# Optimization experiments

Hardware: AMD Instinct MI355X
Metric: run time of the kernel (lower is better)

The kernel has to match this reference:

```python
import jax, jax.numpy as jnp
import numpy as np

N_MEL = 80


def _bce_with_logits(x, t):
    # mean over all elements, numerically stable
    return jnp.mean(jnp.maximum(x, 0.0) - x * t + jnp.log1p(jnp.exp(-jnp.abs(x))))


def _spectral_mel_loss(pred, target):
    w = np.ones(N_MEL, dtype=np.float32)
    w[N_MEL // 4: 3 * N_MEL // 4] *= 1.5
    w[3 * N_MEL // 4:] *= 0.8
    w = jnp.asarray(w)[None, :, None]
    weighted_mse = jnp.mean((pred * w - target * w) ** 2)
    l1 = jnp.mean(jnp.abs(pred - target))
    dp = pred[:, :, 1:] - pred[:, :, :-1]
    dt = target[:, :, 1:] - target[:, :, :-1]
    spectral = jnp.mean((dp - dt) ** 2)
    return weighted_mse + 0.3 * l1 + 0.2 * spectral


def _perceptual_loss(pred, target):
    fw = jnp.exp(-jnp.arange(N_MEL, dtype=jnp.float32) / 20.0)[None, :, None]
    weighted = ((pred - target) ** 2) * fw
    l1 = jnp.mean(jnp.abs(pred - target))
    return jnp.mean(weighted) + 0.5 * l1


def _style_loss(pred, target):
    mean_loss = jnp.mean((jnp.mean(pred, axis=2) - jnp.mean(target, axis=2)) ** 2)
    # torch.var defaults to unbiased (ddof=1)
    var_loss = jnp.mean((jnp.var(pred, axis=2, ddof=1) - jnp.var(target, axis=2, ddof=1)) ** 2)
    c, t = pred.shape[1], pred.shape[2]
    gram_p = jnp.einsum('bct,bdt->bcd', pred, pred) / (c * t)
    gram_t = jnp.einsum('bct,bdt->bcd', target, target) / (c * t)
    gram_loss = jnp.mean((gram_p - gram_t) ** 2)
    return mean_loss + var_loss + 0.5 * gram_loss


def _monotonic_loss(att):
    # att: [B, mel_len, text_len]; vectorized form of the per-step violation loop
    b, mel_len, _ = att.shape
    peaks = jnp.argmax(att, axis=2).astype(jnp.float32)  # [B, mel_len]
    viol = jnp.maximum(peaks[:, :-1] - peaks[:, 1:], 0.0)
    return jnp.sum(viol) / (b * mel_len)


def setup_inputs() -> dict:
    key = jax.random.key(0)
    ks = jax.random.split(key, 6)
    B, C, T, L = 64, N_MEL, 2000, 200
    return {
        'mel_out': jax.random.normal(ks[0], (B, C, T), jnp.float32),
        'mel_out_postnet': jax.random.normal(ks[1], (B, C, T), jnp.float32),
        'mel_target': jax.random.normal(ks[2], (B, C, T), jnp.float32),
        'gate_out': jax.random.normal(ks[3], (B, T), jnp.float32),
        'gate_target': jax.random.uniform(ks[4], (B, T), jnp.float32),
        'attention_weights': jax.random.uniform(ks[5], (B, T, L), jnp.float32),
    }


def reference(mel_out, mel_out_postnet, mel_target, gate_out, gate_target, attention_weights):
    # loss weights (hparams defaults); guide_loss omitted (method truncated in source)
    mel_w, gate_w, spec_w, perc_w, style_w, mono_w = 1.0, 1.0, 0.3, 0.2, 0.1, 0.1
    gate_inner_w = 1.3  # AdaptiveGateLoss initial_weight

    mel_loss = jnp.mean((mel_out - mel_target) ** 2) + jnp.mean((mel_out_postnet - mel_target) ** 2)
    gate_loss = gate_inner_w * _bce_with_logits(gate_out.reshape(-1, 1), gate_target.reshape(-1, 1))
    spectral = _spectral_mel_loss(mel_out_postnet, mel_target)
    perceptual = _perceptual_loss(mel_out_postnet, mel_target)
    style = _style_loss(mel_out_postnet, mel_target)
    mono = _monotonic_loss(attention_weights)

    total = (mel_w * mel_loss + gate_w * gate_loss + spec_w * spectral
             + perc_w * perceptual + style_w * style + mono_w * mono)
    return total
```

## Files before the change

### kernel.cpp

```cpp
#include <hip/hip_runtime.h>
#include <math.h>

#define N_MEL 80
#define B_    64
#define T_    2000
#define L_    200
#define ROWS   (B_*N_MEL)
#define NTOT   (B_*N_MEL*T_)
#define GATE_N (B_*T_)
#define ATT_ROWS (B_*T_)
#define AV_ROWS 64
#define NVIOL  (ATT_ROWS/AV_ROWS)

#define G_MELB   (ROWS/4)
#define G_GATE   64

#define WS_ROWPART 0
#define WS_M8      (WS_ROWPART + ROWS*8)
#define WS_GATEP   (WS_M8 + 8*64*6400)
#define WS_VIOLP   (WS_GATEP + 64)
#define WS_GFP     (WS_VIOLP + NVIOL)

typedef __attribute__((ext_vector_type(8)))  short bf16x8;
typedef __attribute__((ext_vector_type(16))) float f32x16;
typedef unsigned short ush;

__device__ __forceinline__ float blockReduceSum256(float v) {
    __shared__ float red[4];
    #pragma unroll
    for (int off = 32; off; off >>= 1) v += __shfl_down(v, off, 64);
    int lane = threadIdx.x & 63, w = threadIdx.x >> 6;
    if (lane == 0) red[w] = v;
    __syncthreads();
    if (threadIdx.x == 0) v = red[0] + red[1] + red[2] + red[3];
    return v;
}

__device__ __forceinline__ unsigned short f2bf(float f) {
    unsigned u = __float_as_uint(f);
    u = (u + 0x7fffu + ((u >> 16) & 1u)) >> 16;
    return (unsigned short)u;
}

__device__ __forceinline__ void merge4(float& b, int& p) {
    #pragma unroll
    for (int m = 1; m <= 2; m <<= 1) {
        float ob = __shfl_xor(b, m, 64);
        int   op = __shfl_xor(p, m, 64);
        if (ob > b || (ob == b && op < p)) { b = ob; p = op; }
    }
}

__device__ __forceinline__ void scan_sub(const float* __restrict__ rowp, int q,
                                         float& bOut, int& pOut) {
    const float4* rp = (const float4*)rowp;
    float4 v[13];
    #pragma unroll
    for (int i = 0; i < 12; i++) v[i] = rp[q + 4*i];
    v[12] = make_float4(-1.f, -1.f, -1.f, -1.f);
    if (q < 2) v[12] = rp[q + 48];
    float bx=-1.f, by=-1.f, bz=-1.f, bw=-1.f;
    int jx=0, jy=0, jz=0, jw=0;
    #pragma unroll
    for (int i = 0; i < 13; i++) {
        int j = q + 4*i;
        if (v[i].x > bx) { bx = v[i].x; jx = j; }
        if (v[i].y > by) { by = v[i].y; jy = j; }
        if (v[i].z > bz) { bz = v[i].z; jz = j; }
        if (v[i].w > bw) { bw = v[i].w; jw = j; }
    }
    float b = bx; int p = 4*jx;
    if (by > b || (by == b && 4*jy+1 < p)) { b = by; p = 4*jy+1; }
    if (bz > b || (bz == b && 4*jz+2 < p)) { b = bz; p = 4*jz+2; }
    if (bw > b || (bw == b && 4*jw+3 < p)) { b = bw; p = 4*jw+3; }
    bOut = b; pOut = p;
}

__global__ __launch_bounds__(256, 2) void k_melgate(const float* __restrict__ mo,
                                                    const float* __restrict__ mp,
                                                    const float* __restrict__ mt,
                                                    const float* __restrict__ gx,
                                                    const float* __restrict__ gt,
                                                    float* __restrict__ ws) {
    const int bid = blockIdx.x;
    float* rowpart = ws + WS_ROWPART;
    float* gatep   = ws + WS_GATEP;

    if (bid >= G_MELB) {
        const int gb = bid - G_MELB;
        const float4* x4 = (const float4*)gx;
        const float4* t4 = (const float4*)gt;
        float s = 0;
        for (int i = gb*256 + threadIdx.x; i < GATE_N/4; i += G_GATE*256) {
            float4 x = x4[i], t = t4[i];
            float xs[4] = {x.x, x.y, x.z, x.w}, ts[4] = {t.x, t.y, t.z, t.w};
            #pragma unroll
            for (int k = 0; k < 4; k++)
                s += fmaxf(xs[k], 0.0f) - xs[k]*ts[k] + log1pf(expf(-fabsf(xs[k])));
        }
        float tot = blockReduceSum256(s);
        if (threadIdx.x == 0) gatep[gb] = tot;
        return;
    }

    {
        const int wid  = threadIdx.x >> 6;
        const int lane = threadIdx.x & 63;
        const int row  = bid * 4 + wid;
        const long base = (long)row * T_;
        const float4* mo4 = (const float4*)(mo + base);
        const float4* mp4 = (const float4*)(mp + base);
        const float4* mt4 = (const float4*)(mt + base);

        float4 A[8], P[8], Q[8];
        #pragma unroll
        for (int k = 0; k < 7; k++) {
            A[k] = mo4[lane + 64*k];
            P[k] = mp4[lane + 64*k];
            Q[k] = mt4[lane + 64*k];
        }
        const bool t7 = (lane < 52);
        A[7] = make_float4(0.f,0.f,0.f,0.f);
        P[7] = make_float4(0.f,0.f,0.f,0.f);
        Q[7] = make_float4(0.f,0.f,0.f,0.f);
        if (t7) { A[7] = mo4[lane + 448]; P[7] = mp4[lane + 448]; Q[7] = mt4[lane + 448]; }

        float s1=0, s2=0, sl1=0, std_=0, sp=0, sp2=0, st=0, st2=0;
        float carry = 0.f;
        #pragma unroll
        for (int k = 0; k < 8; k++) {
            float4 a = A[k], p = P[k], t = Q[k];
            float e0=a.x-t.x, e1=a.y-t.y, e2=a.z-t.z, e3=a.w-t.w;
            s1 += e0*e0 + e1*e1 + e2*e2 + e3*e3;
            float d0=p.x-t.x, d1=p.y-t.y, d2=p.z-t.z, d3=p.w-t.w;
            s2 += d0*d0 + d1*d1 + d2*d2 + d3*d3;
            sl1 += fabsf(d0) + fabsf(d1) + fabsf(d2) + fabsf(d3);
            sp  += p.x + p.y + p.z + p.w;
            sp2 += p.x*p.x + p.y*p.y + p.z*p.z + p.w*p.w;
            st  += t.x + t.y + t.z + t.w;
            st2 += t.x*t.x + t.y*t.y + t.z*t.z + t.w*t.w;
            float q1 = d1-d0, q2 = d2-d1, q3 = d3-d2;
            std_ += q1*q1 + q2*q2 + q3*q3;
            float pv = __shfl_up(d3, 1, 64);
            if (lane == 0) pv = carry;
            float q0 = d0 - pv;
            bool valid = !(k == 0 && lane == 0) && (k < 7 || t7);
            if (valid) std_ += q0*q0;
            carry = __shfl(d3, 63, 64);
        }

        float vals[8] = {s1, s2, sl1, std_, sp, sp2, st, st2};
        #pragma unroll
        for (int k = 0; k < 8; k++) {
            float v = vals[k];
            #pragma unroll
            for (int off = 32; off; off >>= 1) v += __shfl_down(v, off, 64);
            vals[k] = v;
        }
        if (lane == 0) {
            *(float4*)&rowpart[row*8]     = make_float4(vals[0], vals[1], vals[2], vals[3]);
            *(float4*)&rowpart[row*8 + 4] = make_float4(vals[4], vals[5], vals[6], vals[7]);
        }
    }
}

__global__ __launch_bounds__(192) void k_gram(const float* __restrict__ mp,
                                              const float* __restrict__ mt,
                                              float* __restrict__ M8) {
    const int b  = blockIdx.x >> 3;
    const int kc = blockIdx.x & 7;
    const int k0 = kc * 256;
    const int NS = (kc < 7) ? 16 : 13;

    __shared__ ush Dls[2][96][24];
    __shared__ ush Sls[2][96][24];

    const int tid  = threadIdx.x;
    const int row  = tid >> 1;
    const int half = tid & 1;
    const int lane = tid & 63;
    const int wv   = tid >> 6;
    const long bbase = (long)b * (N_MEL * T_);
    const float* prow = mp + bbase + (long)row * T_ + k0 + half * 8;
    const float* trow = mt + bbase + (long)row * T_ + k0 + half * 8;
    const bool rv = (row < N_MEL);

    f32x16 acc0 = {}, acc1 = {}, acc2 = {};
    float4 pa0, pa1, ta0, ta1;

    auto loadreg = [&](int s) {
        if (rv) {
            pa0 = *(const float4*)(prow + s*16);
            pa1 = *(const float4*)(prow + s*16 + 4);
            ta0 = *(const float4*)(trow + s*16);
            ta1 = *(const float4*)(trow + s*16 + 4);
        } else {
            pa0 = pa1 = ta0 = ta1 = make_float4(0.f, 0.f, 0.f, 0.f);
        }
    };
    auto writelds = [&](int buf) {
        bf16x8 d, s;
        d[0]=f2bf(pa0.x-ta0.x); d[1]=f2bf(pa0.y-ta0.y); d[2]=f2bf(pa0.z-ta0.z); d[3]=f2bf(pa0.w-ta0.w);
        d[4]=f2bf(pa1.x-ta1.x); d[5]=f2bf(pa1.y-ta1.y); d[6]=f2bf(pa1.z-ta1.z); d[7]=f2bf(pa1.w-ta1.w);
        s[0]=f2bf(pa0.x+ta0.x); s[1]=f2bf(pa0.y+ta0.y); s[2]=f2bf(pa0.z+ta0.z); s[3]=f2bf(pa0.w+ta0.w);
        s[4]=f2bf(pa1.x+ta1.x); s[5]=f2bf(pa1.y+ta1.y); s[6]=f2bf(pa1.z+ta1.z); s[7]=f2bf(pa1.w+ta1.w);
        *(bf16x8*)&Dls[buf][row][half*8] = d;
        *(bf16x8*)&Sls[buf][row][half*8] = s;
    };

    loadreg(0);
    writelds(0);
    __syncthreads();

    const int frow = lane & 31;
    const int fkh  = lane >> 5;
    for (int s = 0; s < NS; s++) {
        const int cur = s & 1;
        if (s + 1 < NS) loadreg(s + 1);
        bf16x8 af = *(const bf16x8*)&Dls[cur][wv*32 + frow][fkh*8];
        bf16x8 b0 = *(const bf16x8*)&Sls[cur][      frow][fkh*8];
        bf16x8 b1 = *(const bf16x8*)&Sls[cur][ 32 + frow][fkh*8];
        bf16x8 b2 = *(const bf16x8*)&Sls[cur][ 64 + frow][fkh*8];
        acc0 = __builtin_amdgcn_mfma_f32_32x32x16_bf16(af, b0, acc0, 0, 0, 0);
        acc1 = __builtin_amdgcn_mfma_f32_32x32x16_bf16(af, b1, acc1, 0, 0, 0);
        acc2 = __builtin_amdgcn_mfma_f32_32x32x16_bf16(af, b2, acc2, 0, 0, 0);
        if (s + 1 < NS) writelds((s + 1) & 1);
        __syncthreads();
    }

    float* Mb = M8 + ((long)(kc * B_ + b)) * 6400;
    #pragma unroll
    for (int r = 0; r < 16; r++) {
        int row32 = (r & 3) + 8 * (r >> 2) + 4 * (lane >> 5);
        int c = wv * 32 + row32;
        if (c < N_MEL) {
            Mb[c*80 + frow]      = acc0[r];
            Mb[c*80 + 32 + frow] = acc1[r];
            if (frow < 16) Mb[c*80 + 64 + frow] = acc2[r];
        }
    }
}

__global__ __launch_bounds__(256) void k_gramfin(const float* __restrict__ ws_ro,
                                                 float* __restrict__ gfp) {
    __shared__ float Ms[N_MEL][N_MEL + 1];
    const float* M8 = ws_ro + WS_M8;
    const int b = blockIdx.x;
    const float inv = 1.0f / (float)(N_MEL * T_);

    for (int i = threadIdx.x; i < 6400; i += 256) {
        float m = 0.f;
        #pragma unroll
        for (int kc = 0; kc < 8; kc++)
            m += M8[((long)(kc * B_ + b)) * 6400 + i];
        Ms[i / N_MEL][i % N_MEL] = m;
    }
    __syncthreads();

    float s = 0.f;
    for (int i = threadIdx.x; i < 6400; i += 256) {
        int c = i / N_MEL, d = i % N_MEL;
        float g = 0.5f * (Ms[c][d] + Ms[d][c]) * inv;
        s += g * g;
    }
    float tot = blockReduceSum256(s);
    if (threadIdx.x == 0) gfp[b] = tot;
}

__global__ __launch_bounds__(256, 2) void k_argviol(const float* __restrict__ att,
                                                    float* __restrict__ ws) {
    float* violp = ws + WS_VIOLP;
    __shared__ float pk[AV_ROWS + 1];
    const int ab = blockIdx.x;
    const int g = threadIdx.x >> 2;
    const int q = threadIdx.x & 3;
    const int r0 = ab * AV_ROWS;
    const int r  = r0 + g;

    float b; int p;
    scan_sub(att + (long)r * L_, q, b, p);
    merge4(b, p);
    if (q == 0) pk[g] = (float)p;

    const int rb = r0 + AV_ROWS;
    const bool need_b = ((rb % T_) != 0) && (rb < ATT_ROWS);
    if (g == 0 && need_b) {
        float b2; int p2;
        scan_sub(att + (long)rb * L_, q, b2, p2);
        merge4(b2, p2);
        if (q == 0) pk[AV_ROWS] = (float)p2;
    }
    __syncthreads();

    float s = 0;
    if (threadIdx.x < AV_ROWS) {
        int rr = r0 + threadIdx.x;
        if (((rr + 1) % T_) != 0)
            s = fmaxf(pk[threadIdx.x] - pk[threadIdx.x + 1], 0.0f);
    }
    float tot = blockReduceSum256(s);
    if (threadIdx.x == 0) violp[ab] = tot;
}

__global__ __launch_bounds__(256) void k_final2(const float* __restrict__ ws_ro,
                                                float* __restrict__ out) {
    const float* rowpart = ws_ro + WS_ROWPART;
    const float* gatep   = ws_ro + WS_GATEP;
    const float* violp   = ws_ro + WS_VIOLP;
    const float* gfp     = ws_ro + WS_GFP;

    float a[11] = {0,0,0,0,0,0,0,0,0,0,0};
    for (int row = threadIdx.x; row < ROWS; row += 256) {
        const float4 lo = *(const float4*)(rowpart + row*8);
        const float4 hi = *(const float4*)(rowpart + row*8 + 4);
        int c = row % N_MEL;
        float wc = (c >= 3*N_MEL/4) ? 0.8f : ((c >= N_MEL/4) ? 1.5f : 1.0f);
        float fw = expf(-(float)c / 20.0f);
        a[0] += lo.x;
        a[1] += lo.y;
        a[2] += wc*wc*lo.y;
        a[3] += lo.z;
        a[4] += lo.w;
        a[5] += fw*lo.y;
        float md = (hi.x - hi.z) * (1.0f / T_);
        a[6] += md*md;
        float vp = (hi.y - hi.x*hi.x*(1.0f/T_)) * (1.0f/(T_-1));
        float vt = (hi.w - hi.z*hi.z*(1.0f/T_)) * (1.0f/(T_-1));
        float vd = vp - vt;
        a[7] += vd*vd;
    }
    for (int i = threadIdx.x; i < NVIOL; i += 256) a[9] += violp[i];
    if (threadIdx.x < 64) { a[8] = gatep[threadIdx.x]; a[10] = gfp[threadIdx.x]; }

    __shared__ float red[4][11];
    #pragma unroll
    for (int k = 0; k < 11; k++) {
        float v = a[k];
        #pragma unroll
        for (int off = 32; off; off >>= 1) v += __shfl_down(v, off, 64);
        a[k] = v;
    }
    int lane = threadIdx.x & 63, w = threadIdx.x >> 6;
    if (lane == 0) {
        #pragma unroll
        for (int k = 0; k < 11; k++) red[w][k] = a[k];
    }
    __syncthreads();
    if (threadIdx.x == 0) {
        float r[11];
        #pragma unroll
        for (int k = 0; k < 11; k++) r[k] = red[0][k] + red[1][k] + red[2][k] + red[3][k];
        const float invN = 1.0f / (float)NTOT;
        float mel        = (r[0] + r[1]) * invN;
        float gate       = 1.3f * r[8] / (float)GATE_N;
        float wmse       = r[2] * invN;
        float l1         = r[3] * invN;
        float sdiff      = r[4] / (float)(B_ * N_MEL * (T_ - 1));
        float spectral   = wmse + 0.3f*l1 + 0.2f*sdiff;
        float perceptual = r[5]*invN + 0.5f*l1;
        float mean_loss  = r[6] / (float)ROWS;
        float var_loss   = r[7] / (float)ROWS;
        float gram       = r[10] / (float)(B_ * 6400);
        float style      = mean_loss + var_loss + 0.5f*gram;
        float mono       = r[9] / (float)(B_ * T_);
        out[0] = mel + gate + 0.3f*spectral + 0.2f*perceptual + 0.1f*style + 0.1f*mono;
    }
}

extern "C" void kernel_launch(void* const* d_in, const int* in_sizes, int n_in,
                              void* d_out, int out_size, void* d_ws, size_t ws_size,
                              hipStream_t stream) {
    const float* mo  = (const float*)d_in[0];
    const float* mp  = (const float*)d_in[1];
    const float* mt  = (const float*)d_in[2];
    const float* gx  = (const float*)d_in[3];
    const float* gt  = (const float*)d_in[4];
    const float* att = (const float*)d_in[5];
    float* ws = (float*)d_ws;

    k_melgate<<<G_MELB + G_GATE, 256, 0, stream>>>(mo, mp, mt, gx, gt, ws);
    k_gram   <<<512,  192, 0, stream>>>(mp, mt, ws + WS_M8);
    k_gramfin<<<64,   256, 0, stream>>>(ws, ws + WS_GFP);
    k_argviol<<<NVIOL, 256, 0, stream>>>(att, ws);
    k_final2 <<<1,    256, 0, stream>>>(ws, (float*)d_out);
}
```

Baseline: 94.12 us.

## Fuse mel row statistics into gram MFMA kernel and gate BCE into argmax kernel

Removes the separate mel/gate pass, which read mel_out_postnet and mel_target a second time. The per-row sums are now accumulated inside the gram kernel while its tiles are loaded, and the gate BCE blocks move into the attention argmax launch. Per-chunk row partials go to a new workspace region and are summed in extra blocks of the gram-finalize kernel, which saves one launch and about 2 x 41 MB of HBM reads. In exchange, the gram kernel carries more registers and ALU work per step, and the spectral-difference term needs extra boundary handling across chunks.

```diff
diff --git a/kernel.cpp b/kernel.cpp
--- a/kernel.cpp
+++ b/kernel.cpp
@@ -12,11 +12,9 @@
 #define AV_ROWS 64
 #define NVIOL  (ATT_ROWS/AV_ROWS)
 
-#define G_MELB   (ROWS/4)
-#define G_GATE   64
-
 #define WS_ROWPART 0
-#define WS_M8      (WS_ROWPART + ROWS*8)
+#define WS_ROWCH   (WS_ROWPART + ROWS*8)
+#define WS_M8      (WS_ROWCH + 8*ROWS*8)
 #define WS_GATEP   (WS_M8 + 8*64*6400)
 #define WS_VIOLP   (WS_GATEP + 64)
 #define WS_GFP     (WS_VIOLP + NVIOL)
@@ -76,97 +74,12 @@
     bOut = b; pOut = p;
 }
 
-__global__ __launch_bounds__(256, 2) void k_melgate(const float* __restrict__ mo,
-                                                    const float* __restrict__ mp,
-                                                    const float* __restrict__ mt,
-                                                    const float* __restrict__ gx,
-                                                    const float* __restrict__ gt,
-                                                    float* __restrict__ ws) {
-    const int bid = blockIdx.x;
-    float* rowpart = ws + WS_ROWPART;
-    float* gatep   = ws + WS_GATEP;
-
-    if (bid >= G_MELB) {
-        const int gb = bid - G_MELB;
-        const float4* x4 = (const float4*)gx;
-        const float4* t4 = (const float4*)gt;
-        float s = 0;
-        for (int i = gb*256 + threadIdx.x; i < GATE_N/4; i += G_GATE*256) {
-            float4 x = x4[i], t = t4[i];
-            float xs[4] = {x.x, x.y, x.z, x.w}, ts[4] = {t.x, t.y, t.z, t.w};
-            #pragma unroll
-            for (int k = 0; k < 4; k++)
-                s += fmaxf(xs[k], 0.0f) - xs[k]*ts[k] + log1pf(expf(-fabsf(xs[k])));
-        }
-        float tot = blockReduceSum256(s);
-        if (threadIdx.x == 0) gatep[gb] = tot;
-        return;
-    }
-
-    {
-        const int wid  = threadIdx.x >> 6;
-        const int lane = threadIdx.x & 63;
-        const int row  = bid * 4 + wid;
-        const long base = (long)row * T_;
-        const float4* mo4 = (const float4*)(mo + base);
-        const float4* mp4 = (const float4*)(mp + base);
-        const float4* mt4 = (const float4*)(mt + base);
-
-        float4 A[8], P[8], Q[8];
-        #pragma unroll
-        for (int k = 0; k < 7; k++) {
-            A[k] = mo4[lane + 64*k];
-            P[k] = mp4[lane + 64*k];
-            Q[k] = mt4[lane + 64*k];
-        }
-        const bool t7 = (lane < 52);
-        A[7] = make_float4(0.f,0.f,0.f,0.f);
-        P[7] = make_float4(0.f,0.f,0.f,0.f);
-        Q[7] = make_float4(0.f,0.f,0.f,0.f);
-        if (t7) { A[7] = mo4[lane + 448]; P[7] = mp4[lane + 448]; Q[7] = mt4[lane + 448]; }
-
-        float s1=0, s2=0, sl1=0, std_=0, sp=0, sp2=0, st=0, st2=0;
-        float carry = 0.f;
-        #pragma unroll
-        for (int k = 0; k < 8; k++) {
-            float4 a = A[k], p = P[k], t = Q[k];
-            float e0=a.x-t.x, e1=a.y-t.y, e2=a.z-t.z, e3=a.w-t.w;
-            s1 += e0*e0 + e1*e1 + e2*e2 + e3*e3;
-            float d0=p.x-t.x, d1=p.y-t.y, d2=p.z-t.z, d3=p.w-t.w;
-            s2 += d0*d0 + d1*d1 + d2*d2 + d3*d3;
-            sl1 += fabsf(d0) + fabsf(d1) + fabsf(d2) + fabsf(d3);
-            sp  += p.x + p.y + p.z + p.w;
-            sp2 += p.x*p.x + p.y*p.y + p.z*p.z + p.w*p.w;
-            st  += t.x + t.y + t.z + t.w;
-            st2 += t.x*t.x + t.y*t.y + t.z*t.z + t.w*t.w;
-            float q1 = d1-d0, q2 = d2-d1, q3 = d3-d2;
-            std_ += q1*q1 + q2*q2 + q3*q3;
-            float pv = __shfl_up(d3, 1, 64);
-            if (lane == 0) pv = carry;
-            float q0 = d0 - pv;
-            bool valid = !(k == 0 && lane == 0) && (k < 7 || t7);
-            if (valid) std_ += q0*q0;
-            carry = __shfl(d3, 63, 64);
-        }
-
-        float vals[8] = {s1, s2, sl1, std_, sp, sp2, st, st2};
-        #pragma unroll
-        for (int k = 0; k < 8; k++) {
-            float v = vals[k];
-            #pragma unroll
-            for (int off = 32; off; off >>= 1) v += __shfl_down(v, off, 64);
-            vals[k] = v;
-        }
-        if (lane == 0) {
-            *(float4*)&rowpart[row*8]     = make_float4(vals[0], vals[1], vals[2], vals[3]);
-            *(float4*)&rowpart[row*8 + 4] = make_float4(vals[4], vals[5], vals[6], vals[7]);
-        }
-    }
-}
-
-__global__ __launch_bounds__(192) void k_gram(const float* __restrict__ mp,
-                                              const float* __restrict__ mt,
-                                              float* __restrict__ M8) {
+__global__ __launch_bounds__(192) void k_melgram(const float* __restrict__ mo,
+                                                 const float* __restrict__ mp,
+                                                 const float* __restrict__ mt,
+                                                 float* __restrict__ ws) {
+    float* M8    = ws + WS_M8;
+    float* rowch = ws + WS_ROWCH;
     const int b  = blockIdx.x >> 3;
     const int kc = blockIdx.x & 7;
     const int k0 = kc * 256;
@@ -181,12 +94,23 @@
     const int lane = tid & 63;
     const int wv   = tid >> 6;
     const long bbase = (long)b * (N_MEL * T_);
-    const float* prow = mp + bbase + (long)row * T_ + k0 + half * 8;
-    const float* trow = mt + bbase + (long)row * T_ + k0 + half * 8;
+    const long rbase = bbase + (long)row * T_ + k0 + half * 8;
+    const float* prow = mp + rbase;
+    const float* trow = mt + rbase;
+    const float* orow = mo + rbase;
     const bool rv = (row < N_MEL);
 
     f32x16 acc0 = {}, acc1 = {}, acc2 = {};
-    float4 pa0, pa1, ta0, ta1;
+    float4 pa0, pa1, ta0, ta1, oa0, oa1;
+
+    float s1=0, s2=0, sl1=0, std_=0, sp=0, sp2=0, st=0, st2=0;
+    float saved_plast = 0.f;
+    float edge_d = 0.f;
+    bool  edge_valid = false;
+    if (half == 0 && kc > 0 && rv) {
+        edge_d = mp[rbase - k0 - half*8 + k0 - 1] - mt[rbase - k0 - half*8 + k0 - 1];
+        edge_valid = true;
+    }
 
     auto loadreg = [&](int s) {
         if (rv) {
@@ -194,8 +118,10 @@
             pa1 = *(const float4*)(prow + s*16 + 4);
             ta0 = *(const float4*)(trow + s*16);
             ta1 = *(const float4*)(trow + s*16 + 4);
+            oa0 = *(const float4*)(orow + s*16);
+            oa1 = *(const float4*)(orow + s*16 + 4);
         } else {
-            pa0 = pa1 = ta0 = ta1 = make_float4(0.f, 0.f, 0.f, 0.f);
+            pa0 = pa1 = ta0 = ta1 = oa0 = oa1 = make_float4(0.f, 0.f, 0.f, 0.f);
         }
     };
     auto writelds = [&](int buf) {
@@ -207,9 +133,40 @@
         *(bf16x8*)&Dls[buf][row][half*8] = d;
         *(bf16x8*)&Sls[buf][row][half*8] = s;
     };
+    auto accum = [&](int s) {
+        float pv[8] = {pa0.x,pa0.y,pa0.z,pa0.w,pa1.x,pa1.y,pa1.z,pa1.w};
+        float tv[8] = {ta0.x,ta0.y,ta0.z,ta0.w,ta1.x,ta1.y,ta1.z,ta1.w};
+        float ov[8] = {oa0.x,oa0.y,oa0.z,oa0.w,oa1.x,oa1.y,oa1.z,oa1.w};
+        float d[8];
+        float ls1=0, ls2=0, lsl=0, lstd=0, lsp=0, lsp2=0, lst=0, lst2=0;
+        #pragma unroll
+        for (int i = 0; i < 8; i++) {
+            float e = ov[i] - tv[i];
+            ls1 += e*e;
+            d[i] = pv[i] - tv[i];
+            ls2 += d[i]*d[i];
+            lsl += fabsf(d[i]);
+            lsp += pv[i]; lsp2 += pv[i]*pv[i];
+            lst += tv[i]; lst2 += tv[i]*tv[i];
+        }
+        #pragma unroll
+        for (int i = 1; i < 8; i++) { float q = d[i]-d[i-1]; lstd += q*q; }
+        float plast = __shfl_xor(d[7], 1, 64);
+        float prev; bool bvalid;
+        if (half == 1) { prev = plast; bvalid = true; }
+        else if (s == 0) { prev = edge_d; bvalid = edge_valid; }
+        else { prev = saved_plast; bvalid = true; }
+        if (bvalid) { float q0 = d[0] - prev; lstd += q0*q0; }
+        saved_plast = plast;
+        if (rv) {
+            s1+=ls1; s2+=ls2; sl1+=lsl; std_+=lstd;
+            sp+=lsp; sp2+=lsp2; st+=lst; st2+=lst2;
+        }
+    };
 
     loadreg(0);
     writelds(0);
+    accum(0);
     __syncthreads();
 
     const int frow = lane & 31;
@@ -224,7 +181,7 @@
         acc0 = __builtin_amdgcn_mfma_f32_32x32x16_bf16(af, b0, acc0, 0, 0, 0);
         acc1 = __builtin_amdgcn_mfma_f32_32x32x16_bf16(af, b1, acc1, 0, 0, 0);
         acc2 = __builtin_amdgcn_mfma_f32_32x32x16_bf16(af, b2, acc2, 0, 0, 0);
-        if (s + 1 < NS) writelds((s + 1) & 1);
+        if (s + 1 < NS) { writelds((s + 1) & 1); accum(s + 1); }
         __syncthreads();
     }
 
@@ -239,37 +196,41 @@
             if (frow < 16) Mb[c*80 + 64 + frow] = acc2[r];
         }
     }
-}
-
-__global__ __launch_bounds__(256) void k_gramfin(const float* __restrict__ ws_ro,
-                                                 float* __restrict__ gfp) {
-    __shared__ float Ms[N_MEL][N_MEL + 1];
-    const float* M8 = ws_ro + WS_M8;
-    const int b = blockIdx.x;
-    const float inv = 1.0f / (float)(N_MEL * T_);
-
-    for (int i = threadIdx.x; i < 6400; i += 256) {
-        float m = 0.f;
-        #pragma unroll
-        for (int kc = 0; kc < 8; kc++)
-            m += M8[((long)(kc * B_ + b)) * 6400 + i];
-        Ms[i / N_MEL][i % N_MEL] = m;
-    }
-    __syncthreads();
-
-    float s = 0.f;
-    for (int i = threadIdx.x; i < 6400; i += 256) {
-        int c = i / N_MEL, d = i % N_MEL;
-        float g = 0.5f * (Ms[c][d] + Ms[d][c]) * inv;
-        s += g * g;
-    }
-    float tot = blockReduceSum256(s);
-    if (threadIdx.x == 0) gfp[b] = tot;
+
+    float vals[8] = {s1, s2, sl1, std_, sp, sp2, st, st2};
+    #pragma unroll
+    for (int k = 0; k < 8; k++) vals[k] += __shfl_xor(vals[k], 1, 64);
+    if (half == 0 && rv) {
+        float* rc = rowch + ((long)(kc * ROWS) + (b * N_MEL + row)) * 8;
+        *(float4*)rc       = make_float4(vals[0], vals[1], vals[2], vals[3]);
+        *(float4*)(rc + 4) = make_float4(vals[4], vals[5], vals[6], vals[7]);
+    }
 }
 
 __global__ __launch_bounds__(256, 2) void k_argviol(const float* __restrict__ att,
+                                                    const float* __restrict__ gx,
+                                                    const float* __restrict__ gt,
                                                     float* __restrict__ ws) {
     float* violp = ws + WS_VIOLP;
+    float* gatep = ws + WS_GATEP;
+
+    if (blockIdx.x >= NVIOL) {
+        const int gb = blockIdx.x - NVIOL;
+        const float4* x4 = (const float4*)gx;
+        const float4* t4 = (const float4*)gt;
+        float s = 0;
+        for (int i = gb*256 + threadIdx.x; i < GATE_N/4; i += 64*256) {
+            float4 x = x4[i], t = t4[i];
+            float xs[4] = {x.x, x.y, x.z, x.w}, ts[4] = {t.x, t.y, t.z, t.w};
+            #pragma unroll
+            for (int k = 0; k < 4; k++)
+                s += fmaxf(xs[k], 0.0f) - xs[k]*ts[k] + log1pf(expf(-fabsf(xs[k])));
+        }
+        float tot = blockReduceSum256(s);
+        if (threadIdx.x == 0) gatep[gb] = tot;
+        return;
+    }
+
     __shared__ float pk[AV_ROWS + 1];
     const int ab = blockIdx.x;
     const int g = threadIdx.x >> 2;
@@ -300,6 +261,51 @@
     }
     float tot = blockReduceSum256(s);
     if (threadIdx.x == 0) violp[ab] = tot;
+}
+
+__global__ __launch_bounds__(256) void k_gramfin(const float* __restrict__ ws_ro,
+                                                 float* __restrict__ ws_out) {
+    if (blockIdx.x >= 64) {
+        const float* rowch = ws_ro + WS_ROWCH;
+        float* rowpart = ws_out + WS_ROWPART;
+        int r = (blockIdx.x - 64) * 256 + threadIdx.x;
+        float4 lo = make_float4(0.f,0.f,0.f,0.f), hi = lo;
+        #pragma unroll
+        for (int kc = 0; kc < 8; kc++) {
+            const float* rc = rowch + ((long)(kc * ROWS) + r) * 8;
+            float4 a = *(const float4*)rc;
+            float4 c = *(const float4*)(rc + 4);
+            lo.x += a.x; lo.y += a.y; lo.z += a.z; lo.w += a.w;
+            hi.x += c.x; hi.y += c.y; hi.z += c.z; hi.w += c.w;
+        }
+        *(float4*)&rowpart[r*8]     = lo;
+        *(float4*)&rowpart[r*8 + 4] = hi;
+        return;
+    }
+
+    __shared__ float Ms[N_MEL][N_MEL + 1];
+    const float* M8 = ws_ro + WS_M8;
+    float* gfp = ws_out + WS_GFP;
+    const int b = blockIdx.x;
+    const float inv = 1.0f / (float)(N_MEL * T_);
+
+    for (int i = threadIdx.x; i < 6400; i += 256) {
+        float m = 0.f;
+        #pragma unroll
+        for (int kc = 0; kc < 8; kc++)
+            m += M8[((long)(kc * B_ + b)) * 6400 + i];
+        Ms[i / N_MEL][i % N_MEL] = m;
+    }
+    __syncthreads();
+
+    float s = 0.f;
+    for (int i = threadIdx.x; i < 6400; i += 256) {
+        int c = i / N_MEL, d = i % N_MEL;
+        float g = 0.5f * (Ms[c][d] + Ms[d][c]) * inv;
+        s += g * g;
+    }
+    float tot = blockReduceSum256(s);
+    if (threadIdx.x == 0) gfp[b] = tot;
 }
 
 __global__ __launch_bounds__(256) void k_final2(const float* __restrict__ ws_ro,
@@ -378,9 +384,8 @@
     const float* att = (const float*)d_in[5];
     float* ws = (float*)d_ws;
 
-    k_melgate<<<G_MELB + G_GATE, 256, 0, stream>>>(mo, mp, mt, gx, gt, ws);
-    k_gram   <<<512,  192, 0, stream>>>(mp, mt, ws + WS_M8);
-    k_gramfin<<<64,   256, 0, stream>>>(ws, ws + WS_GFP);
-    k_argviol<<<NVIOL, 256, 0, stream>>>(att, ws);
-    k_final2 <<<1,    256, 0, stream>>>(ws, (float*)d_out);
-}
+    k_melgram<<<512,        192, 0, stream>>>(mo, mp, mt, ws);
+    k_argviol<<<NVIOL + 64, 256, 0, stream>>>(att, gx, gt, ws);
+    k_gramfin<<<84,         256, 0, stream>>>(ws, ws);
+    k_final2 <<<1,          256, 0, stream>>>(ws, (float*)d_out);
+}
```

After: 91.58 us. -2.7%, faster.
